# Kernel optimization log

Measured on AMD Instinct MI355X. Metric: run time of the kernel, lower is better.

The kernel has to match this reference:

```python
import jax, jax.numpy as jnp
import numpy as np

B, S, T, D = 32, 128, 65536, 768
VOCAB, N_SEC, N_TEMP, N_NEG, MAX_SENT, N_TS = 30522, 6, 3, 2, 128, 512
LN_EPS = 1e-5


def setup_inputs() -> dict:
    key = jax.random.key(0)
    ks = jax.random.split(key, 16)
    return {
        "token_ids": jax.random.randint(ks[0], (T,), 0, VOCAB),
        "segment_ids": jnp.sort(jax.random.randint(ks[1], (T,), 0, B * S)),
        "section_ids": jax.random.randint(ks[2], (B, S), 0, N_SEC),
        "temporality_ids": jax.random.randint(ks[3], (B, S), 0, N_TEMP),
        "negation_ids": jax.random.randint(ks[4], (B, S), 0, N_NEG),
        "position_ids": jax.random.randint(ks[5], (B, S), 0, MAX_SENT),
        "timestamp_ids": jax.random.randint(ks[6], (B, S), 0, N_TS),
        "token_table": jax.random.normal(ks[7], (VOCAB, D), jnp.float32),
        "section_table": jax.random.normal(ks[8], (N_SEC, D), jnp.float32),
        "temporality_table": jax.random.normal(ks[9], (N_TEMP, D), jnp.float32),
        "negation_table": jax.random.normal(ks[10], (N_NEG, D), jnp.float32),
        "position_table": jax.random.normal(ks[11], (MAX_SENT, D), jnp.float32),
        "timestamp_table": jax.random.normal(ks[12], (N_TS, D), jnp.float32),
        "ln_gamma": jnp.ones((D,), jnp.float32),
        "ln_beta": jnp.zeros((D,), jnp.float32),
        "proj_w": jax.random.normal(ks[13], (D, D), jnp.float32) * (1.0 / np.sqrt(D)),
        "proj_b": jnp.zeros((D,), jnp.float32),
    }


def reference(token_ids, segment_ids, section_ids, temporality_ids, negation_ids,
              position_ids, timestamp_ids, token_table, section_table,
              temporality_table, negation_table, position_table, timestamp_table,
              ln_gamma, ln_beta, proj_w, proj_b):
    # ragged per-sentence token-embedding mean pool (segment mean over B*S slots)
    tok = token_table[token_ids]                                  # [T, D]
    sums = jax.ops.segment_sum(tok, segment_ids, num_segments=B * S)
    cnt = jax.ops.segment_sum(jnp.ones((T,), tok.dtype), segment_ids,
                              num_segments=B * S)
    base = (sums / jnp.maximum(cnt, 1.0)[:, None]).reshape(B, S, D)
    # multi-embedding sum
    enriched = (base
                + section_table[section_ids]
                + temporality_table[temporality_ids]
                + negation_table[negation_ids]
                + position_table[position_ids]
                + timestamp_table[timestamp_ids])                 # [B, S, D]
    # LayerNorm + Linear
    mu = enriched.mean(-1, keepdims=True)
    var = jnp.mean(jnp.square(enriched - mu), axis=-1, keepdims=True)
    normed = (enriched - mu) * jax.lax.rsqrt(var + LN_EPS) * ln_gamma + ln_beta
    tokens = jnp.einsum('bsd,ed->bse', normed, proj_w) + proj_b   # [B, S, D]
    padding_mask = jnp.zeros((B, S), dtype=bool)                  # all sentences valid
    return tokens, padding_mask
```

## Files before the change

kernel.cpp:

```cpp
#include <hip/hip_runtime.h>
#include <stdint.h>

#define Tn 65536
#define Dn 768
#define NSEG 4096
#define NWBLK 576
#define NMBLK 16

typedef __bf16 bf16;
typedef __bf16 bf16x8 __attribute__((ext_vector_type(8)));
typedef float f32x4 __attribute__((ext_vector_type(4)));

__device__ inline void f4add(float4& a, const float4& v) {
  a.x += v.x; a.y += v.y; a.z += v.z; a.w += v.w;
}

__global__ __launch_bounds__(256) void k_prep(
    const int* __restrict__ seg, int* __restrict__ starts)
{
  const int t = blockIdx.x * 256 + threadIdx.x;
  const int s = seg[t];
  const int sp = (t == 0) ? -1 : seg[t - 1];
  for (int k = sp + 1; k <= s; ++k) starts[k] = t;
  if (t == Tn - 1)
    for (int k = s + 1; k <= NSEG; ++k) starts[k] = Tn;
}

__global__ void k_pool_ln(
    const int* __restrict__ token_ids, const int* __restrict__ starts,
    const int* __restrict__ section_ids, const int* __restrict__ temporality_ids,
    const int* __restrict__ negation_ids, const int* __restrict__ position_ids,
    const int* __restrict__ timestamp_ids,
    const float* __restrict__ token_table, const float* __restrict__ section_table,
    const float* __restrict__ temporality_table, const float* __restrict__ negation_table,
    const float* __restrict__ position_table, const float* __restrict__ timestamp_table,
    const float* __restrict__ gamma, const float* __restrict__ beta,
    bf16* __restrict__ out_normed,
    const float* __restrict__ proj_w, bf16* __restrict__ wb,
    float* __restrict__ mask_out)
{
  const int n = blockIdx.x;
  const int lane = threadIdx.x;

  if (n >= NSEG) {
    if (n < NSEG + NWBLK) {
      const int base = ((n - NSEG) * 64 + lane) * 4;
      #pragma unroll
      for (int u = 0; u < 4; ++u) {
        const float4 v = ((const float4*)proj_w)[base + u];
        alignas(8) bf16 o[4] = {(bf16)v.x, (bf16)v.y, (bf16)v.z, (bf16)v.w};
        ((ushort4*)wb)[base + u] = *(ushort4*)o;
      }
    } else {
      ((float4*)mask_out)[(n - NSEG - NWBLK) * 64 + lane] =
          make_float4(0.f, 0.f, 0.f, 0.f);
    }
    return;
  }

  const int start = starts[n];
  const int end   = starts[n + 1];
  const float scale = 1.0f / fmaxf((float)(end - start), 1.0f);

  const float4* tt = (const float4*)token_table;

  const float4* e1 = (const float4*)(section_table     + (size_t)section_ids[n]     * Dn);
  const float4* e2 = (const float4*)(temporality_table + (size_t)temporality_ids[n] * Dn);
  const float4* e3 = (const float4*)(negation_table    + (size_t)negation_ids[n]    * Dn);
  const float4* e4 = (const float4*)(position_table    + (size_t)position_ids[n]    * Dn);
  const float4* e5 = (const float4*)(timestamp_table   + (size_t)timestamp_ids[n]   * Dn);
  float4 en[3];
  #pragma unroll
  for (int j = 0; j < 3; ++j) {
    const int d = j * 64 + lane;
    float4 q = e1[d];
    f4add(q, e2[d]); f4add(q, e3[d]); f4add(q, e4[d]); f4add(q, e5[d]);
    en[j] = q;
  }

  float4 acc[3];
  #pragma unroll
  for (int j = 0; j < 3; ++j) acc[j] = make_float4(0.f, 0.f, 0.f, 0.f);

  int t = start;
  int ids[8];
  #pragma unroll
  for (int u = 0; u < 8; ++u)
    ids[u] = token_ids[(t + u < Tn) ? t + u : Tn - 1];

  while (t + 8 <= end) {
    float4 L[8][3];
    #pragma unroll
    for (int u = 0; u < 8; ++u) {
      const float4* r = tt + (size_t)ids[u] * 192;
      #pragma unroll
      for (int j = 0; j < 3; ++j) L[u][j] = r[j * 64 + lane];
    }
    t += 8;
    #pragma unroll
    for (int u = 0; u < 8; ++u)
      ids[u] = token_ids[(t + u < Tn) ? t + u : Tn - 1];
    #pragma unroll
    for (int j = 0; j < 3; ++j) {
      f4add(L[0][j], L[1][j]); f4add(L[2][j], L[3][j]);
      f4add(L[4][j], L[5][j]); f4add(L[6][j], L[7][j]);
      f4add(L[0][j], L[2][j]); f4add(L[4][j], L[6][j]);
      f4add(L[0][j], L[4][j]); f4add(acc[j], L[0][j]);
    }
  }
  for (int u = 0; t < end; ++t, ++u) {
    const float4* r = tt + (size_t)ids[u] * 192;
    #pragma unroll
    for (int j = 0; j < 3; ++j) f4add(acc[j], r[j * 64 + lane]);
  }

  float4 e[3];
  #pragma unroll
  for (int j = 0; j < 3; ++j) {
    e[j].x = acc[j].x * scale + en[j].x;
    e[j].y = acc[j].y * scale + en[j].y;
    e[j].z = acc[j].z * scale + en[j].z;
    e[j].w = acc[j].w * scale + en[j].w;
  }

  float s = 0.f;
  #pragma unroll
  for (int j = 0; j < 3; ++j) s += e[j].x + e[j].y + e[j].z + e[j].w;
  #pragma unroll
  for (int o = 32; o > 0; o >>= 1) s += __shfl_xor(s, o, 64);
  const float mu = s * (1.0f / 768.0f);

  float v = 0.f;
  #pragma unroll
  for (int j = 0; j < 3; ++j) {
    e[j].x -= mu; e[j].y -= mu; e[j].z -= mu; e[j].w -= mu;
    v += e[j].x * e[j].x + e[j].y * e[j].y + e[j].z * e[j].z + e[j].w * e[j].w;
  }
  #pragma unroll
  for (int o = 32; o > 0; o >>= 1) v += __shfl_xor(v, o, 64);
  const float inv = rsqrtf(v * (1.0f / 768.0f) + 1e-5f);

  #pragma unroll
  for (int j = 0; j < 3; ++j) {
    const int d = j * 64 + lane;
    const float4 g = ((const float4*)gamma)[d];
    const float4 b = ((const float4*)beta)[d];
    alignas(8) bf16 o[4];
    o[0] = (bf16)(e[j].x * inv * g.x + b.x);
    o[1] = (bf16)(e[j].y * inv * g.y + b.y);
    o[2] = (bf16)(e[j].z * inv * g.z + b.z);
    o[3] = (bf16)(e[j].w * inv * g.w + b.w);
    *(ushort4*)(out_normed + (size_t)n * Dn + 4 * d) = *(ushort4*)o;
  }
}

__global__ __launch_bounds__(256) void k_gemm(
    const bf16* __restrict__ A, const bf16* __restrict__ W,
    const float* __restrict__ bias, float* __restrict__ out)
{
  __shared__ bf16 As[128 * 32];
  __shared__ bf16 Bs[128 * 32];
  const int tid  = threadIdx.x;
  const int lane = tid & 63;
  const int w    = tid >> 6;
  const int m0 = blockIdx.y * 128;
  const int n0 = blockIdx.x * 128;
  const int wm = (w >> 1) * 64;
  const int wn = (w & 1) * 64;

  f32x4 acc[4][4];
  #pragma unroll
  for (int i = 0; i < 4; ++i)
    #pragma unroll
    for (int j = 0; j < 4; ++j) acc[i][j] = (f32x4){0.f, 0.f, 0.f, 0.f};

  const int sr = tid >> 2;
  const int sc = (tid & 3) * 8;
  const bf16* a0 = A + (size_t)(m0 + sr) * 768 + sc;
  const bf16* a1 = a0 + (size_t)64 * 768;
  const bf16* b0 = W + (size_t)(n0 + sr) * 768 + sc;
  const bf16* b1 = b0 + (size_t)64 * 768;

  for (int kt = 0; kt < 24; ++kt) {
    const int ko = kt * 32;
    __syncthreads();
    __builtin_amdgcn_global_load_lds(
        (const __attribute__((address_space(1))) void*)(a0 + ko),
        (__attribute__((address_space(3))) void*)(As + tid * 8), 16, 0, 0);
    __builtin_amdgcn_global_load_lds(
        (const __attribute__((address_space(1))) void*)(a1 + ko),
        (__attribute__((address_space(3))) void*)(As + (256 + tid) * 8), 16, 0, 0);
    __builtin_amdgcn_global_load_lds(
        (const __attribute__((address_space(1))) void*)(b0 + ko),
        (__attribute__((address_space(3))) void*)(Bs + tid * 8), 16, 0, 0);
    __builtin_amdgcn_global_load_lds(
        (const __attribute__((address_space(1))) void*)(b1 + ko),
        (__attribute__((address_space(3))) void*)(Bs + (256 + tid) * 8), 16, 0, 0);
    __syncthreads();

    bf16x8 af[4], bfr[4];
    #pragma unroll
    for (int i = 0; i < 4; ++i)
      af[i] = *(const bf16x8*)(As + (wm + i * 16 + (lane & 15)) * 32 + (lane >> 4) * 8);
    #pragma unroll
    for (int j = 0; j < 4; ++j)
      bfr[j] = *(const bf16x8*)(Bs + (wn + j * 16 + (lane & 15)) * 32 + (lane >> 4) * 8);

    #pragma unroll
    for (int i = 0; i < 4; ++i)
      #pragma unroll
      for (int j = 0; j < 4; ++j)
        acc[i][j] = __builtin_amdgcn_mfma_f32_16x16x32_bf16(af[i], bfr[j], acc[i][j], 0, 0, 0);
  }

  float bvals[4];
  #pragma unroll
  for (int j = 0; j < 4; ++j) bvals[j] = bias[n0 + wn + j * 16 + (lane & 15)];
  const int r0 = (lane >> 4) * 4;
  #pragma unroll
  for (int i = 0; i < 4; ++i) {
    #pragma unroll
    for (int r = 0; r < 4; ++r) {
      const int gm = m0 + wm + i * 16 + r0 + r;
      float* orow = out + (size_t)gm * 768 + n0 + wn;
      #pragma unroll
      for (int j = 0; j < 4; ++j)
        orow[j * 16 + (lane & 15)] = acc[i][j][r] + bvals[j];
    }
  }
}

extern "C" void kernel_launch(void* const* d_in, const int* in_sizes, int n_in,
                              void* d_out, int out_size, void* d_ws, size_t ws_size,
                              hipStream_t stream) {
  const int* token_ids       = (const int*)d_in[0];
  const int* segment_ids     = (const int*)d_in[1];
  const int* section_ids     = (const int*)d_in[2];
  const int* temporality_ids = (const int*)d_in[3];
  const int* negation_ids    = (const int*)d_in[4];
  const int* position_ids    = (const int*)d_in[5];
  const int* timestamp_ids   = (const int*)d_in[6];
  const float* token_table       = (const float*)d_in[7];
  const float* section_table     = (const float*)d_in[8];
  const float* temporality_table = (const float*)d_in[9];
  const float* negation_table    = (const float*)d_in[10];
  const float* position_table    = (const float*)d_in[11];
  const float* timestamp_table   = (const float*)d_in[12];
  const float* ln_gamma = (const float*)d_in[13];
  const float* ln_beta  = (const float*)d_in[14];
  const float* proj_w   = (const float*)d_in[15];
  const float* proj_b   = (const float*)d_in[16];

  float* out = (float*)d_out;
  bf16* wsW = (bf16*)d_ws;
  bf16* wsN = wsW + (size_t)Dn * Dn;
  int*  wsS = (int*)((char*)d_ws + (size_t)(Dn * Dn + NSEG * Dn) * 2);

  k_prep<<<256, 256, 0, stream>>>(segment_ids, wsS);
  k_pool_ln<<<NSEG + NWBLK + NMBLK, 64, 0, stream>>>(token_ids, wsS, section_ids,
      temporality_ids, negation_ids, position_ids, timestamp_ids,
      token_table, section_table, temporality_table, negation_table,
      position_table, timestamp_table, ln_gamma, ln_beta, wsN,
      proj_w, wsW, out + (size_t)NSEG * Dn);
  k_gemm<<<dim3(6, 32), 256, 0, stream>>>(wsN, wsW, proj_b, out);
}
```

Baseline: 204.7 us.

## Drop prep kernel via in-block binary search and split pooling across two waves

Removes the separate segment-start kernel launch; each pooling block now finds its segment bounds by binary searching the sorted segment ids, one search per wave. Blocks grow to two wavefronts that each sum half of the segment's tokens, then combine the partial sums through shared memory before the LayerNorm tail runs on wave 0. This cuts one launch and doubles the memory-level parallelism per segment, at the cost of redundant log(T) global reads per block, a block barrier, and a wave sitting idle during the LayerNorm.

```diff
diff --git a/kernel.cpp b/kernel.cpp
--- a/kernel.cpp
+++ b/kernel.cpp
@@ -5,7 +5,7 @@
 #define Dn 768
 #define NSEG 4096
 #define NWBLK 576
-#define NMBLK 16
+#define NMBLK 8
 
 typedef __bf16 bf16;
 typedef __bf16 bf16x8 __attribute__((ext_vector_type(8)));
@@ -15,19 +15,8 @@
   a.x += v.x; a.y += v.y; a.z += v.z; a.w += v.w;
 }
 
-__global__ __launch_bounds__(256) void k_prep(
-    const int* __restrict__ seg, int* __restrict__ starts)
-{
-  const int t = blockIdx.x * 256 + threadIdx.x;
-  const int s = seg[t];
-  const int sp = (t == 0) ? -1 : seg[t - 1];
-  for (int k = sp + 1; k <= s; ++k) starts[k] = t;
-  if (t == Tn - 1)
-    for (int k = s + 1; k <= NSEG; ++k) starts[k] = Tn;
-}
-
 __global__ void k_pool_ln(
-    const int* __restrict__ token_ids, const int* __restrict__ starts,
+    const int* __restrict__ token_ids, const int* __restrict__ seg,
     const int* __restrict__ section_ids, const int* __restrict__ temporality_ids,
     const int* __restrict__ negation_ids, const int* __restrict__ position_ids,
     const int* __restrict__ timestamp_ids,
@@ -39,56 +28,78 @@
     const float* __restrict__ proj_w, bf16* __restrict__ wb,
     float* __restrict__ mask_out)
 {
-  const int n = blockIdx.x;
-  const int lane = threadIdx.x;
+  const int n    = blockIdx.x;
+  const int tid  = threadIdx.x;
+  const int lane = tid & 63;
+  const int w    = tid >> 6;
 
   if (n >= NSEG) {
     if (n < NSEG + NWBLK) {
-      const int base = ((n - NSEG) * 64 + lane) * 4;
-      #pragma unroll
-      for (int u = 0; u < 4; ++u) {
+      const int base = ((n - NSEG) * 128 + tid) * 2;
+      #pragma unroll
+      for (int u = 0; u < 2; ++u) {
         const float4 v = ((const float4*)proj_w)[base + u];
         alignas(8) bf16 o[4] = {(bf16)v.x, (bf16)v.y, (bf16)v.z, (bf16)v.w};
         ((ushort4*)wb)[base + u] = *(ushort4*)o;
       }
     } else {
-      ((float4*)mask_out)[(n - NSEG - NWBLK) * 64 + lane] =
+      ((float4*)mask_out)[(n - NSEG - NWBLK) * 128 + tid] =
           make_float4(0.f, 0.f, 0.f, 0.f);
     }
     return;
   }
 
-  const int start = starts[n];
-  const int end   = starts[n + 1];
-  const float scale = 1.0f / fmaxf((float)(end - start), 1.0f);
+  __shared__ int sb[2];
+  __shared__ float4 red[3][64];
+
+  {
+    int lo = 0, hi = Tn;
+    const int tgt = n + w;
+    while (lo < hi) {
+      const int mid = (lo + hi) >> 1;
+      if (seg[mid] < tgt) lo = mid + 1; else hi = mid;
+    }
+    if (lane == 0) sb[w] = lo;
+  }
+  __syncthreads();
+  const int start = sb[0];
+  const int end   = sb[1];
+  const int len   = end - start;
+  const float scale = 1.0f / fmaxf((float)len, 1.0f);
+
+  const int half = (len + 1) >> 1;
+  const int ws = start + w * half;
+  const int we = w ? end : start + half;
 
   const float4* tt = (const float4*)token_table;
 
-  const float4* e1 = (const float4*)(section_table     + (size_t)section_ids[n]     * Dn);
-  const float4* e2 = (const float4*)(temporality_table + (size_t)temporality_ids[n] * Dn);
-  const float4* e3 = (const float4*)(negation_table    + (size_t)negation_ids[n]    * Dn);
-  const float4* e4 = (const float4*)(position_table    + (size_t)position_ids[n]    * Dn);
-  const float4* e5 = (const float4*)(timestamp_table   + (size_t)timestamp_ids[n]   * Dn);
   float4 en[3];
-  #pragma unroll
-  for (int j = 0; j < 3; ++j) {
-    const int d = j * 64 + lane;
-    float4 q = e1[d];
-    f4add(q, e2[d]); f4add(q, e3[d]); f4add(q, e4[d]); f4add(q, e5[d]);
-    en[j] = q;
+  if (w == 0) {
+    const float4* e1 = (const float4*)(section_table     + (size_t)section_ids[n]     * Dn);
+    const float4* e2 = (const float4*)(temporality_table + (size_t)temporality_ids[n] * Dn);
+    const float4* e3 = (const float4*)(negation_table    + (size_t)negation_ids[n]    * Dn);
+    const float4* e4 = (const float4*)(position_table    + (size_t)position_ids[n]    * Dn);
+    const float4* e5 = (const float4*)(timestamp_table   + (size_t)timestamp_ids[n]   * Dn);
+    #pragma unroll
+    for (int j = 0; j < 3; ++j) {
+      const int d = j * 64 + lane;
+      float4 q = e1[d];
+      f4add(q, e2[d]); f4add(q, e3[d]); f4add(q, e4[d]); f4add(q, e5[d]);
+      en[j] = q;
+    }
   }
 
   float4 acc[3];
   #pragma unroll
   for (int j = 0; j < 3; ++j) acc[j] = make_float4(0.f, 0.f, 0.f, 0.f);
 
-  int t = start;
+  int t = ws;
   int ids[8];
   #pragma unroll
   for (int u = 0; u < 8; ++u)
     ids[u] = token_ids[(t + u < Tn) ? t + u : Tn - 1];
 
-  while (t + 8 <= end) {
+  while (t < we) {
     float4 L[8][3];
     #pragma unroll
     for (int u = 0; u < 8; ++u) {
@@ -96,23 +107,38 @@
       #pragma unroll
       for (int j = 0; j < 3; ++j) L[u][j] = r[j * 64 + lane];
     }
+    const int nb = we - t;
     t += 8;
     #pragma unroll
     for (int u = 0; u < 8; ++u)
       ids[u] = token_ids[(t + u < Tn) ? t + u : Tn - 1];
-    #pragma unroll
-    for (int j = 0; j < 3; ++j) {
-      f4add(L[0][j], L[1][j]); f4add(L[2][j], L[3][j]);
-      f4add(L[4][j], L[5][j]); f4add(L[6][j], L[7][j]);
-      f4add(L[0][j], L[2][j]); f4add(L[4][j], L[6][j]);
-      f4add(L[0][j], L[4][j]); f4add(acc[j], L[0][j]);
-    }
-  }
-  for (int u = 0; t < end; ++t, ++u) {
-    const float4* r = tt + (size_t)ids[u] * 192;
-    #pragma unroll
-    for (int j = 0; j < 3; ++j) f4add(acc[j], r[j * 64 + lane]);
-  }
+    if (nb >= 8) {
+      #pragma unroll
+      for (int j = 0; j < 3; ++j) {
+        f4add(L[0][j], L[1][j]); f4add(L[2][j], L[3][j]);
+        f4add(L[4][j], L[5][j]); f4add(L[6][j], L[7][j]);
+        f4add(L[0][j], L[2][j]); f4add(L[4][j], L[6][j]);
+        f4add(L[0][j], L[4][j]); f4add(acc[j], L[0][j]);
+      }
+    } else {
+      #pragma unroll
+      for (int u = 0; u < 8; ++u) {
+        if (u < nb) {
+          #pragma unroll
+          for (int j = 0; j < 3; ++j) f4add(acc[j], L[u][j]);
+        }
+      }
+    }
+  }
+
+  if (w == 1) {
+    #pragma unroll
+    for (int j = 0; j < 3; ++j) red[j][lane] = acc[j];
+  }
+  __syncthreads();
+  if (w == 1) return;
+  #pragma unroll
+  for (int j = 0; j < 3; ++j) f4add(acc[j], red[j][lane]);
 
   float4 e[3];
   #pragma unroll
@@ -254,11 +280,9 @@
   float* out = (float*)d_out;
   bf16* wsW = (bf16*)d_ws;
   bf16* wsN = wsW + (size_t)Dn * Dn;
-  int*  wsS = (int*)((char*)d_ws + (size_t)(Dn * Dn + NSEG * Dn) * 2);
-
-  k_prep<<<256, 256, 0, stream>>>(segment_ids, wsS);
-  k_pool_ln<<<NSEG + NWBLK + NMBLK, 64, 0, stream>>>(token_ids, wsS, section_ids,
-      temporality_ids, negation_ids, position_ids, timestamp_ids,
+
+  k_pool_ln<<<NSEG + NWBLK + NMBLK, 128, 0, stream>>>(token_ids, segment_ids,
+      section_ids, temporality_ids, negation_ids, position_ids, timestamp_ids,
       token_table, section_table, temporality_table, negation_table,
       position_table, timestamp_table, ln_gamma, ln_beta, wsN,
       proj_w, wsW, out + (size_t)NSEG * Dn);
```

Result: slower. 222.1 us (+8.5%).
